# Kernel optimization log

Measured on AMD Instinct MI355X. Metric: run time of the kernel, lower is better.

## Reference

```python
import jax, jax.numpy as jnp
import numpy as np

B, H, D = 8, 1024, 4
K_COUP = 1.0
DT = 1.0


def setup_inputs() -> dict:
    key = jax.random.key(0)
    k1, k2, k3, k4, k5 = jax.random.split(key, 5)
    return {
        "theta_prev": jax.random.normal(k1, (B, H, D), dtype=jnp.float32),
        "gamma": jax.random.normal(k2, (B, H), dtype=jnp.float32),
        "A": jax.random.normal(k3, (B, H, H), dtype=jnp.float32),
        "omega": jax.random.normal(k4, (H, D), dtype=jnp.float32) * 0.1,
        "kappa": jnp.ones((H, D), dtype=jnp.float32),
        "alpha": jax.random.normal(k5, (H, H), dtype=jnp.float32) * 0.1,
    }


def reference(theta_prev, gamma, A, omega, kappa, alpha):
    # theta_prev: [B,H,D], gamma: [B,H], A: [B,H,H]
    Bn, Hn, Dn = theta_prev.shape
    # symmetrize + relu lateral coupling matrix
    A_lat = jax.nn.relu(0.5 * (A + jnp.swapaxes(A, 1, 2)))  # [B,H,H]
    # pairwise phase differences: theta_j - theta_i - alpha -> [B,H,H,D]
    phase_diff = (theta_prev[:, None, :, :] - theta_prev[:, :, None, :]
                  - alpha[None, :, :, None])
    # weighted sum over j axis
    coupling = (K_COUP / Hn) * jnp.sum(A_lat[..., None] * jnp.sin(phase_diff), axis=2)  # [B,H,D]
    theta_dot = omega[None] + coupling + kappa[None] * (gamma[..., None] - theta_prev)
    return theta_prev + DT * theta_dot
```

## Files before the change

kernel.cpp:

```cpp
#include <hip/hip_runtime.h>
#include <math.h>

#define BB 8
#define HH 1024
#define DD 4
#define TI 16
#define NJC 8
#define JC (HH / NJC)


__global__ __launch_bounds__(256, 8) void kuramoto_partial(
    const float* __restrict__ theta, const float* __restrict__ A,
    const float* __restrict__ alpha, float* __restrict__ ws)
{
    const int blk = blockIdx.x;
    const int jc  = blk & (NJC - 1);
    const int it  = (blk >> 3) & 63;
    const int b   = blk >> 9;
    const int i0  = it * TI;
    const int j0  = jc * JC;
    const int t   = threadIdx.x;
    const int ti  = t >> 4;
    const int tj  = t & 15;

    __shared__ float sTh0[JC], sTh1[JC], sTh2[JC], sTh3[JC];
    __shared__ float sAT[JC][TI + 1];

    const float* Ab = A + (size_t)b * HH * HH;

    if (t < JC) {
        const float4 v = ((const float4*)theta)[(size_t)b * HH + j0 + t];
        sTh0[t] = v.x; sTh1[t] = v.y; sTh2[t] = v.z; sTh3[t] = v.w;
    }

    {
        const int r = t >> 2;
        const int c = (t & 3) * 4;
        #pragma unroll
        for (int rr = 0; rr < JC; rr += 64) {
            const int row = rr + r;
            const float4 v = *(const float4*)&Ab[(size_t)(j0 + row) * HH + i0 + c];
            sAT[row][c + 0] = v.x;
            sAT[row][c + 1] = v.y;
            sAT[row][c + 2] = v.z;
            sAT[row][c + 3] = v.w;
        }
    }
    __syncthreads();

    const float4 thi = ((const float4*)theta)[(size_t)b * HH + i0 + ti];
    const float4* Arow4  = (const float4*)(Ab    + (size_t)(i0 + ti) * HH + j0);
    const float4* alrow4 = (const float4*)(alpha + (size_t)(i0 + ti) * HH + j0);

    float a0 = 0.f, a1 = 0.f, a2 = 0.f, a3 = 0.f;

    #pragma unroll
    for (int s = 0; s < JC / 64; ++s) {
        const int q = tj + 16 * s;
        const float4 ad = Arow4[q];
        const float4 al = alrow4[q];
        const int j = 4 * q;
        #pragma unroll
        for (int k = 0; k < 4; ++k) {
            const float adk = (&ad.x)[k];
            const float alk = (&al.x)[k];
            const float at  = sAT[j + k][ti];
            const float alat = fmaxf(0.5f * (adk + at), 0.0f);
            a0 += alat * __sinf(sTh0[j + k] - thi.x - alk);
            a1 += alat * __sinf(sTh1[j + k] - thi.y - alk);
            a2 += alat * __sinf(sTh2[j + k] - thi.z - alk);
            a3 += alat * __sinf(sTh3[j + k] - thi.w - alk);
        }
    }

    #pragma unroll
    for (int off = 8; off >= 1; off >>= 1) {
        a0 += __shfl_down(a0, off, 16);
        a1 += __shfl_down(a1, off, 16);
        a2 += __shfl_down(a2, off, 16);
        a3 += __shfl_down(a3, off, 16);
    }

    if (tj == 0) {
        float4 r; r.x = a0; r.y = a1; r.z = a2; r.w = a3;
        ((float4*)ws)[((size_t)jc * BB + b) * HH + i0 + ti] = r;
    }
}

__global__ __launch_bounds__(256) void kuramoto_final(
    const float* __restrict__ theta, const float* __restrict__ gamma,
    const float* __restrict__ omega, const float* __restrict__ kappa,
    const float* __restrict__ ws, float* __restrict__ out)
{
    const int idx = blockIdx.x * 256 + threadIdx.x;
    const int i   = idx & (HH - 1);
    const float4* w4 = (const float4*)ws;

    float4 p = w4[idx];
    #pragma unroll
    for (int jc = 1; jc < NJC; ++jc) {
        const float4 q = w4[(size_t)jc * BB * HH + idx];
        p.x += q.x; p.y += q.y; p.z += q.z; p.w += q.w;
    }

    const float4 th = ((const float4*)theta)[idx];
    const float4 om = ((const float4*)omega)[i];
    const float4 kp = ((const float4*)kappa)[i];
    const float  g  = gamma[idx];
    const float  inv = 1.0f / HH;

    float4 o;
    o.x = th.x + om.x + p.x * inv + kp.x * (g - th.x);
    o.y = th.y + om.y + p.y * inv + kp.y * (g - th.y);
    o.z = th.z + om.z + p.z * inv + kp.z * (g - th.z);
    o.w = th.w + om.w + p.w * inv + kp.w * (g - th.w);
    ((float4*)out)[idx] = o;
}

extern "C" void kernel_launch(void* const* d_in, const int* in_sizes, int n_in,
                              void* d_out, int out_size, void* d_ws, size_t ws_size,
                              hipStream_t stream) {
    const float* theta = (const float*)d_in[0];
    const float* gamma = (const float*)d_in[1];
    const float* A     = (const float*)d_in[2];
    const float* omega = (const float*)d_in[3];
    const float* kappa = (const float*)d_in[4];
    const float* alpha = (const float*)d_in[5];
    float* out = (float*)d_out;
    float* ws  = (float*)d_ws;

    hipLaunchKernelGGL(kuramoto_partial, dim3(BB * (HH / TI) * NJC), dim3(256), 0, stream,
                       theta, A, alpha, ws);
    hipLaunchKernelGGL(kuramoto_final, dim3(BB * HH / 256), dim3(256), 0, stream,
                       theta, gamma, omega, kappa, ws, out);
}
```

Before: 94.08 us.

## Fuse partial and final kernels with double-buffered A-transpose tiles and native sin

Merges the split-j partial kernel and the reduction/epilogue kernel into one kernel where each 512-thread block covers all j for 16 rows. The workspace round trip and second launch go away. The A-transpose column tiles are double-buffered in shared memory and prefetched while the current tile is computed. Phases are pre-scaled by 1/(2π) so the hardware sin instruction can be called directly. This cuts the grid to 512 blocks, which lowers parallelism and adds a barrier per chunk.

```diff
diff --git a/kernel.cpp b/kernel.cpp
--- a/kernel.cpp
+++ b/kernel.cpp
@@ -3,118 +3,118 @@
 
 #define BB 8
 #define HH 1024
-#define DD 4
 #define TI 16
-#define NJC 8
-#define JC (HH / NJC)
+#define JC 128
+#define NJC (HH / JC)
+#define C2PI 0.15915494309189535f
 
+#define SA_K   545
+#define SA_BUF (4 * SA_K)
 
-__global__ __launch_bounds__(256, 8) void kuramoto_partial(
-    const float* __restrict__ theta, const float* __restrict__ A,
-    const float* __restrict__ alpha, float* __restrict__ ws)
+__global__ __launch_bounds__(512, 4) void kuramoto_fused(
+    const float* __restrict__ theta, const float* __restrict__ gamma,
+    const float* __restrict__ A, const float* __restrict__ omega,
+    const float* __restrict__ kappa, const float* __restrict__ alpha,
+    float* __restrict__ out)
 {
     const int blk = blockIdx.x;
-    const int jc  = blk & (NJC - 1);
-    const int it  = (blk >> 3) & 63;
-    const int b   = blk >> 9;
+    const int it  = blk & 63;
+    const int b   = blk >> 6;
     const int i0  = it * TI;
-    const int j0  = jc * JC;
     const int t   = threadIdx.x;
-    const int ti  = t >> 4;
-    const int tj  = t & 15;
+    const int ti  = t >> 5;
+    const int tj  = t & 31;
 
-    __shared__ float sTh0[JC], sTh1[JC], sTh2[JC], sTh3[JC];
-    __shared__ float sAT[JC][TI + 1];
+    __shared__ float4 sTh4[HH];
+    __shared__ float  sA[2 * SA_BUF];
 
     const float* Ab = A + (size_t)b * HH * HH;
 
-    if (t < JC) {
-        const float4 v = ((const float4*)theta)[(size_t)b * HH + j0 + t];
-        sTh0[t] = v.x; sTh1[t] = v.y; sTh2[t] = v.z; sTh3[t] = v.w;
+    #pragma unroll
+    for (int r = 0; r < 2; ++r) {
+        const int j = t + 512 * r;
+        float4 v = ((const float4*)theta)[(size_t)b * HH + j];
+        v.x *= C2PI; v.y *= C2PI; v.z *= C2PI; v.w *= C2PI;
+        sTh4[(j & 3) * 256 + (j >> 2)] = v;
     }
 
+    const int sr = t >> 2;
+    const int sc = (t & 3) * 4;
+    const float* colbase = Ab + (size_t)i0 + sc;
     {
-        const int r = t >> 2;
-        const int c = (t & 3) * 4;
-        #pragma unroll
-        for (int rr = 0; rr < JC; rr += 64) {
-            const int row = rr + r;
-            const float4 v = *(const float4*)&Ab[(size_t)(j0 + row) * HH + i0 + c];
-            sAT[row][c + 0] = v.x;
-            sAT[row][c + 1] = v.y;
-            sAT[row][c + 2] = v.z;
-            sAT[row][c + 3] = v.w;
-        }
+        const float4 v = *(const float4*)&colbase[(size_t)sr * HH];
+        float* dst = &sA[(sr & 3) * SA_K + (sr >> 2) * 17 + sc];
+        dst[0] = v.x; dst[1] = v.y; dst[2] = v.z; dst[3] = v.w;
     }
+
+    const int i = i0 + ti;
+    const float4 thi = ((const float4*)theta)[(size_t)b * HH + i];
+    const float tix = thi.x * C2PI, tiy = thi.y * C2PI,
+                tiz = thi.z * C2PI, tiw = thi.w * C2PI;
+
+    const float4* Arow4 = (const float4*)(Ab    + (size_t)i * HH);
+    const float4* Al4   = (const float4*)(alpha + (size_t)i * HH);
+
+    float4 ad = Arow4[tj];
+    float4 al = Al4[tj];
+
     __syncthreads();
-
-    const float4 thi = ((const float4*)theta)[(size_t)b * HH + i0 + ti];
-    const float4* Arow4  = (const float4*)(Ab    + (size_t)(i0 + ti) * HH + j0);
-    const float4* alrow4 = (const float4*)(alpha + (size_t)(i0 + ti) * HH + j0);
 
     float a0 = 0.f, a1 = 0.f, a2 = 0.f, a3 = 0.f;
 
-    #pragma unroll
-    for (int s = 0; s < JC / 64; ++s) {
-        const int q = tj + 16 * s;
-        const float4 ad = Arow4[q];
-        const float4 al = alrow4[q];
-        const int j = 4 * q;
+    #pragma unroll 2
+    for (int jc = 0; jc < NJC; ++jc) {
+        const int buf = (jc & 1) ? SA_BUF : 0;
+        const bool more = (jc + 1 < NJC);
+        float4 adn, aln, vn;
+        if (more) {
+            adn = Arow4[32 * (jc + 1) + tj];
+            aln = Al4  [32 * (jc + 1) + tj];
+            vn  = *(const float4*)&colbase[(size_t)(JC * (jc + 1) + sr) * HH];
+        }
+
+        const float* sa = sA + buf + tj * 17 + ti;
+        const int tb = 32 * jc + tj;
         #pragma unroll
         for (int k = 0; k < 4; ++k) {
-            const float adk = (&ad.x)[k];
-            const float alk = (&al.x)[k];
-            const float at  = sAT[j + k][ti];
-            const float alat = fmaxf(0.5f * (adk + at), 0.0f);
-            a0 += alat * __sinf(sTh0[j + k] - thi.x - alk);
-            a1 += alat * __sinf(sTh1[j + k] - thi.y - alk);
-            a2 += alat * __sinf(sTh2[j + k] - thi.z - alk);
-            a3 += alat * __sinf(sTh3[j + k] - thi.w - alk);
+            const float  at   = sa[k * SA_K];
+            const float  alat = fmaxf(0.5f * ((&ad.x)[k] + at), 0.0f);
+            const float  alc  = (&al.x)[k] * C2PI;
+            const float4 tjv  = sTh4[k * 256 + tb];
+            a0 += alat * __builtin_amdgcn_sinf(tjv.x - (tix + alc));
+            a1 += alat * __builtin_amdgcn_sinf(tjv.y - (tiy + alc));
+            a2 += alat * __builtin_amdgcn_sinf(tjv.z - (tiz + alc));
+            a3 += alat * __builtin_amdgcn_sinf(tjv.w - (tiw + alc));
         }
+
+        if (more) {
+            float* dst = &sA[(buf ^ SA_BUF) + (sr & 3) * SA_K + (sr >> 2) * 17 + sc];
+            dst[0] = vn.x; dst[1] = vn.y; dst[2] = vn.z; dst[3] = vn.w;
+            ad = adn; al = aln;
+        }
+        __syncthreads();
     }
 
     #pragma unroll
-    for (int off = 8; off >= 1; off >>= 1) {
-        a0 += __shfl_down(a0, off, 16);
-        a1 += __shfl_down(a1, off, 16);
-        a2 += __shfl_down(a2, off, 16);
-        a3 += __shfl_down(a3, off, 16);
+    for (int off = 16; off >= 1; off >>= 1) {
+        a0 += __shfl_down(a0, off, 32);
+        a1 += __shfl_down(a1, off, 32);
+        a2 += __shfl_down(a2, off, 32);
+        a3 += __shfl_down(a3, off, 32);
     }
 
     if (tj == 0) {
-        float4 r; r.x = a0; r.y = a1; r.z = a2; r.w = a3;
-        ((float4*)ws)[((size_t)jc * BB + b) * HH + i0 + ti] = r;
+        const float4 om = ((const float4*)omega)[i];
+        const float4 kp = ((const float4*)kappa)[i];
+        const float  g  = gamma[(size_t)b * HH + i];
+        const float  inv = 1.0f / HH;
+        float4 o;
+        o.x = thi.x + om.x + a0 * inv + kp.x * (g - thi.x);
+        o.y = thi.y + om.y + a1 * inv + kp.y * (g - thi.y);
+        o.z = thi.z + om.z + a2 * inv + kp.z * (g - thi.z);
+        o.w = thi.w + om.w + a3 * inv + kp.w * (g - thi.w);
+        ((float4*)out)[(size_t)b * HH + i] = o;
     }
-}
-
-__global__ __launch_bounds__(256) void kuramoto_final(
-    const float* __restrict__ theta, const float* __restrict__ gamma,
-    const float* __restrict__ omega, const float* __restrict__ kappa,
-    const float* __restrict__ ws, float* __restrict__ out)
-{
-    const int idx = blockIdx.x * 256 + threadIdx.x;
-    const int i   = idx & (HH - 1);
-    const float4* w4 = (const float4*)ws;
-
-    float4 p = w4[idx];
-    #pragma unroll
-    for (int jc = 1; jc < NJC; ++jc) {
-        const float4 q = w4[(size_t)jc * BB * HH + idx];
-        p.x += q.x; p.y += q.y; p.z += q.z; p.w += q.w;
-    }
-
-    const float4 th = ((const float4*)theta)[idx];
-    const float4 om = ((const float4*)omega)[i];
-    const float4 kp = ((const float4*)kappa)[i];
-    const float  g  = gamma[idx];
-    const float  inv = 1.0f / HH;
-
-    float4 o;
-    o.x = th.x + om.x + p.x * inv + kp.x * (g - th.x);
-    o.y = th.y + om.y + p.y * inv + kp.y * (g - th.y);
-    o.z = th.z + om.z + p.z * inv + kp.z * (g - th.z);
-    o.w = th.w + om.w + p.w * inv + kp.w * (g - th.w);
-    ((float4*)out)[idx] = o;
 }
 
 extern "C" void kernel_launch(void* const* d_in, const int* in_sizes, int n_in,
@@ -127,10 +127,8 @@
     const float* kappa = (const float*)d_in[4];
     const float* alpha = (const float*)d_in[5];
     float* out = (float*)d_out;
-    float* ws  = (float*)d_ws;
+    (void)d_ws; (void)ws_size;
 
-    hipLaunchKernelGGL(kuramoto_partial, dim3(BB * (HH / TI) * NJC), dim3(256), 0, stream,
-                       theta, A, alpha, ws);
-    hipLaunchKernelGGL(kuramoto_final, dim3(BB * HH / 256), dim3(256), 0, stream,
-                       theta, gamma, omega, kappa, ws, out);
+    hipLaunchKernelGGL(kuramoto_fused, dim3(BB * (HH / TI)), dim3(512), 0, stream,
+                       theta, gamma, A, omega, kappa, alpha, out);
 }
```

Result: slower. 99.82 us (+6.1%).

## Process symmetric tile pairs of A once and use raw hardware sin

Applied to the files above, without the earlier changes.

The partial kernel now assigns each block a pair of 64x64 tiles (P,Q) from the upper triangle and loads A's tile and its transpose once. It computes the symmetrized ReLU coupling in shared memory and then runs two passes, one per orientation, so each A element is read from global memory once instead of twice. Theta and alpha are pre-scaled by 1/(2π) so the raw v_sin builtin can be used, and per-tile partials are written to a 16-slot workspace that the final kernel sums. The cost is a serial loop to decode the triangular index, an uneven workload between diagonal and off-diagonal blocks, and lower occupancy from the larger shared-memory and register footprint.

```diff
diff --git a/kernel.cpp b/kernel.cpp
--- a/kernel.cpp
+++ b/kernel.cpp
@@ -3,88 +3,161 @@
 
 #define BB 8
 #define HH 1024
-#define DD 4
-#define TI 16
-#define NJC 8
-#define JC (HH / NJC)
-
-
-__global__ __launch_bounds__(256, 8) void kuramoto_partial(
+#define TT 64
+#define NT (HH / TT)
+#define NOFF ((NT * (NT - 1)) / 2)
+#define NPAIR (NOFF + NT)
+#define LDP 68
+#define C2PI 0.15915494309189535f
+
+
+__device__ __forceinline__ void do_pass(
+    const float* __restrict__ lat,
+    const float4* __restrict__ thRow,
+    const float4* __restrict__ thCol,
+    const float* __restrict__ alpha,
+    int arow0, int acol0,
+    float4* __restrict__ ws4,
+    size_t wsSlotBase,
+    int tr, int tc)
+{
+    float acc[4][4];
+    #pragma unroll
+    for (int k = 0; k < 4; ++k)
+        #pragma unroll
+        for (int d = 0; d < 4; ++d) acc[k][d] = 0.f;
+
+    float4 thq[4];
+    #pragma unroll
+    for (int m = 0; m < 4; ++m) thq[m] = thCol[4 * tc + m];
+
+    #pragma unroll
+    for (int k = 0; k < 4; ++k) {
+        const int r = tr + 16 * k;
+        const float4 thp  = thRow[r];
+        const float4 lat4 = *(const float4*)&lat[r * LDP + 4 * tc];
+        const float4 al4  = *(const float4*)&alpha[(size_t)(arow0 + r) * HH + acol0 + 4 * tc];
+        #pragma unroll
+        for (int m = 0; m < 4; ++m) {
+            const float lm  = (&lat4.x)[m];
+            const float alc = (&al4.x)[m] * C2PI;
+            const float4 tq = thq[m];
+            acc[k][0] += lm * __builtin_amdgcn_sinf(tq.x - thp.x - alc);
+            acc[k][1] += lm * __builtin_amdgcn_sinf(tq.y - thp.y - alc);
+            acc[k][2] += lm * __builtin_amdgcn_sinf(tq.z - thp.z - alc);
+            acc[k][3] += lm * __builtin_amdgcn_sinf(tq.w - thp.w - alc);
+        }
+    }
+
+    #pragma unroll
+    for (int off = 8; off >= 1; off >>= 1)
+        #pragma unroll
+        for (int k = 0; k < 4; ++k)
+            #pragma unroll
+            for (int d = 0; d < 4; ++d)
+                acc[k][d] += __shfl_down(acc[k][d], off, 16);
+
+    if (tc == 0) {
+        #pragma unroll
+        for (int k = 0; k < 4; ++k) {
+            float4 r4;
+            r4.x = acc[k][0]; r4.y = acc[k][1]; r4.z = acc[k][2]; r4.w = acc[k][3];
+            ws4[wsSlotBase + tr + 16 * k] = r4;
+        }
+    }
+}
+
+__global__ __launch_bounds__(256, 4) void kuramoto_partial(
     const float* __restrict__ theta, const float* __restrict__ A,
     const float* __restrict__ alpha, float* __restrict__ ws)
 {
+    __shared__ float  sLat [TT * LDP];
+    __shared__ float  sLatT[TT * LDP];
+    __shared__ float4 sThP[TT], sThQ[TT];
+
     const int blk = blockIdx.x;
-    const int jc  = blk & (NJC - 1);
-    const int it  = (blk >> 3) & 63;
-    const int b   = blk >> 9;
-    const int i0  = it * TI;
-    const int j0  = jc * JC;
-    const int t   = threadIdx.x;
-    const int ti  = t >> 4;
-    const int tj  = t & 15;
-
-    __shared__ float sTh0[JC], sTh1[JC], sTh2[JC], sTh3[JC];
-    __shared__ float sAT[JC][TI + 1];
+    const int b   = blk / NPAIR;
+    const int p   = blk - b * NPAIR;
+    int P, Q;
+    if (p < NOFF) {
+        int pp = p, row = 0;
+        while (pp >= NT - 1 - row) { pp -= NT - 1 - row; ++row; }
+        P = row; Q = row + 1 + pp;
+    } else {
+        P = Q = p - NOFF;
+    }
+    const bool diag = (P == Q);
+    const int p0 = P * TT, q0 = Q * TT;
+
+    const int t  = threadIdx.x;
+    const int tr = t >> 4;
+    const int tc = t & 15;
+    const int rr = t >> 2;
+    const int cs = (t & 3) * 16;
 
     const float* Ab = A + (size_t)b * HH * HH;
 
-    if (t < JC) {
-        const float4 v = ((const float4*)theta)[(size_t)b * HH + j0 + t];
-        sTh0[t] = v.x; sTh1[t] = v.y; sTh2[t] = v.z; sTh3[t] = v.w;
-    }
-
     {
-        const int r = t >> 2;
-        const int c = (t & 3) * 4;
-        #pragma unroll
-        for (int rr = 0; rr < JC; rr += 64) {
-            const int row = rr + r;
-            const float4 v = *(const float4*)&Ab[(size_t)(j0 + row) * HH + i0 + c];
-            sAT[row][c + 0] = v.x;
-            sAT[row][c + 1] = v.y;
-            sAT[row][c + 2] = v.z;
-            sAT[row][c + 3] = v.w;
-        }
+        const float* gA = Ab + (size_t)(p0 + rr) * HH + q0 + cs;
+        float* dst = &sLat[rr * LDP + cs];
+        #pragma unroll
+        for (int q = 0; q < 4; ++q)
+            *(float4*)&dst[4 * q] = *(const float4*)&gA[4 * q];
+    }
+    if (!diag) {
+        const float* gB = Ab + (size_t)(q0 + rr) * HH + p0 + cs;
+        float* dst = &sLatT[rr * LDP + cs];
+        #pragma unroll
+        for (int q = 0; q < 4; ++q)
+            *(float4*)&dst[4 * q] = *(const float4*)&gB[4 * q];
+    }
+    if (t < TT) {
+        float4 v = ((const float4*)theta)[(size_t)b * HH + p0 + t];
+        v.x *= C2PI; v.y *= C2PI; v.z *= C2PI; v.w *= C2PI;
+        sThP[t] = v;
+    } else if (t < 2 * TT) {
+        const int u = t - TT;
+        float4 v = ((const float4*)theta)[(size_t)b * HH + q0 + u];
+        v.x *= C2PI; v.y *= C2PI; v.z *= C2PI; v.w *= C2PI;
+        sThQ[u] = v;
     }
     __syncthreads();
 
-    const float4 thi = ((const float4*)theta)[(size_t)b * HH + i0 + ti];
-    const float4* Arow4  = (const float4*)(Ab    + (size_t)(i0 + ti) * HH + j0);
-    const float4* alrow4 = (const float4*)(alpha + (size_t)(i0 + ti) * HH + j0);
-
-    float a0 = 0.f, a1 = 0.f, a2 = 0.f, a3 = 0.f;
-
-    #pragma unroll
-    for (int s = 0; s < JC / 64; ++s) {
-        const int q = tj + 16 * s;
-        const float4 ad = Arow4[q];
-        const float4 al = alrow4[q];
-        const int j = 4 * q;
-        #pragma unroll
-        for (int k = 0; k < 4; ++k) {
-            const float adk = (&ad.x)[k];
-            const float alk = (&al.x)[k];
-            const float at  = sAT[j + k][ti];
-            const float alat = fmaxf(0.5f * (adk + at), 0.0f);
-            a0 += alat * __sinf(sTh0[j + k] - thi.x - alk);
-            a1 += alat * __sinf(sTh1[j + k] - thi.y - alk);
-            a2 += alat * __sinf(sTh2[j + k] - thi.z - alk);
-            a3 += alat * __sinf(sTh3[j + k] - thi.w - alk);
-        }
-    }
-
-    #pragma unroll
-    for (int off = 8; off >= 1; off >>= 1) {
-        a0 += __shfl_down(a0, off, 16);
-        a1 += __shfl_down(a1, off, 16);
-        a2 += __shfl_down(a2, off, 16);
-        a3 += __shfl_down(a3, off, 16);
-    }
-
-    if (tj == 0) {
-        float4 r; r.x = a0; r.y = a1; r.z = a2; r.w = a3;
-        ((float4*)ws)[((size_t)jc * BB + b) * HH + i0 + ti] = r;
-    }
+    if (!diag) {
+        float lv[16];
+        #pragma unroll
+        for (int e = 0; e < 16; ++e) {
+            const int c = cs + e;
+            lv[e] = fmaxf(0.5f * (sLat[rr * LDP + c] + sLatT[c * LDP + rr]), 0.0f);
+        }
+        #pragma unroll
+        for (int e = 0; e < 16; ++e) {
+            const int c = cs + e;
+            sLat [rr * LDP + c]  = lv[e];
+            sLatT[c * LDP + rr]  = lv[e];
+        }
+    } else {
+        float lv[16];
+        #pragma unroll
+        for (int e = 0; e < 16; ++e) {
+            const int c = cs + e;
+            lv[e] = fmaxf(0.5f * (sLat[rr * LDP + c] + sLat[c * LDP + rr]), 0.0f);
+        }
+        __syncthreads();
+        #pragma unroll
+        for (int e = 0; e < 16; ++e)
+            sLat[rr * LDP + cs + e] = lv[e];
+    }
+    __syncthreads();
+
+    float4* ws4 = (float4*)ws;
+
+    do_pass(sLat, sThP, sThQ, alpha, p0, q0, ws4,
+            (size_t)(b * NT + Q) * HH + p0, tr, tc);
+
+    if (!diag)
+        do_pass(sLatT, sThQ, sThP, alpha, q0, p0, ws4,
+                (size_t)(b * NT + P) * HH + q0, tr, tc);
 }
 
 __global__ __launch_bounds__(256) void kuramoto_final(
@@ -94,13 +167,14 @@
 {
     const int idx = blockIdx.x * 256 + threadIdx.x;
     const int i   = idx & (HH - 1);
+    const int b   = idx >> 10;
     const float4* w4 = (const float4*)ws;
 
-    float4 p = w4[idx];
-    #pragma unroll
-    for (int jc = 1; jc < NJC; ++jc) {
-        const float4 q = w4[(size_t)jc * BB * HH + idx];
-        p.x += q.x; p.y += q.y; p.z += q.z; p.w += q.w;
+    float4 psum = w4[((size_t)b * NT) * HH + i];
+    #pragma unroll
+    for (int o = 1; o < NT; ++o) {
+        const float4 q = w4[((size_t)b * NT + o) * HH + i];
+        psum.x += q.x; psum.y += q.y; psum.z += q.z; psum.w += q.w;
     }
 
     const float4 th = ((const float4*)theta)[idx];
@@ -110,10 +184,10 @@
     const float  inv = 1.0f / HH;
 
     float4 o;
-    o.x = th.x + om.x + p.x * inv + kp.x * (g - th.x);
-    o.y = th.y + om.y + p.y * inv + kp.y * (g - th.y);
-    o.z = th.z + om.z + p.z * inv + kp.z * (g - th.z);
-    o.w = th.w + om.w + p.w * inv + kp.w * (g - th.w);
+    o.x = th.x + om.x + psum.x * inv + kp.x * (g - th.x);
+    o.y = th.y + om.y + psum.y * inv + kp.y * (g - th.y);
+    o.z = th.z + om.z + psum.z * inv + kp.z * (g - th.z);
+    o.w = th.w + om.w + psum.w * inv + kp.w * (g - th.w);
     ((float4*)out)[idx] = o;
 }
 
@@ -129,7 +203,7 @@
     float* out = (float*)d_out;
     float* ws  = (float*)d_ws;
 
-    hipLaunchKernelGGL(kuramoto_partial, dim3(BB * (HH / TI) * NJC), dim3(256), 0, stream,
+    hipLaunchKernelGGL(kuramoto_partial, dim3(BB * NPAIR), dim3(256), 0, stream,
                        theta, A, alpha, ws);
     hipLaunchKernelGGL(kuramoto_final, dim3(BB * HH / 256), dim3(256), 0, stream,
                        theta, gamma, omega, kappa, ws, out);
```

Result: slower. 102.5 us (+8.9%).
